# Performance work log

Hardware: AMD Instinct MI355X
Metric: run time of the kernel (lower is better)

Reference implementation:

```python
import jax, jax.numpy as jnp
import numpy as np


def setup_inputs() -> dict:
    key = jax.random.key(0)
    k1, k2, k3 = jax.random.split(key, 3)
    B, n, d = 8, 2048, 128
    x = jax.random.normal(k1, (B, n, d), dtype=jnp.float32)
    adj = jax.random.uniform(k2, (B, n, n), dtype=jnp.float32)
    # nn.Linear(2*d, 1): weight [1, 2d], bias [1]. Store weight flat [2d], bias scalar.
    bound = 1.0 / np.sqrt(2 * d)
    W = jax.random.uniform(k3, (2 * d,), dtype=jnp.float32, minval=-bound, maxval=bound)
    b = jnp.zeros((), dtype=jnp.float32)
    return {"x": x, "adj": adj, "W": W, "b": b}


def reference(x, adj, W, b):
    # linear(cat(x_i, x_j)) == x_i @ W_left + x_j @ W_right + b
    d = x.shape[-1]
    w_left, w_right = W[:d], W[d:]
    s_left = jnp.einsum('bnd,d->bn', x, w_left)   # [B, n]
    s_right = jnp.einsum('bnd,d->bn', x, w_right)  # [B, n]
    att = jax.nn.sigmoid(s_left[:, :, None] + s_right[:, None, :] + b)  # [B, n, n]
    return att * adj
```

## Files before the change

kernel.cpp:

```cpp
#include <hip/hip_runtime.h>
#include <math.h>

#define BATCH 8
#define NN 2048
#define DD 128

__global__ __launch_bounds__(256) void score_kernel(
    const float* __restrict__ x, const float* __restrict__ W,
    const float* __restrict__ bias,
    float* __restrict__ sl, float* __restrict__ sr) {
    int wave = (blockIdx.x * blockDim.x + threadIdx.x) >> 6;
    int lane = threadIdx.x & 63;
    if (wave >= BATCH * NN) return;
    const float* xr = x + (size_t)wave * DD;
    float x0 = xr[lane];
    float x1 = xr[lane + 64];
    float l = x0 * W[lane] + x1 * W[lane + 64];
    float r = x0 * W[DD + lane] + x1 * W[DD + lane + 64];
    #pragma unroll
    for (int off = 32; off; off >>= 1) {
        l += __shfl_xor(l, off, 64);
        r += __shfl_xor(r, off, 64);
    }
    if (lane == 0) {
        sl[wave] = l + bias[0];
        sr[wave] = r;
    }
}

__global__ __launch_bounds__(256) void att_kernel(
    const float* __restrict__ adj, const float* __restrict__ sl,
    const float* __restrict__ sr, float* __restrict__ out) {
    const long total = (long)BATCH * NN * (NN / 4);
    long stride = (long)gridDim.x * blockDim.x;
    for (long e = (long)blockIdx.x * blockDim.x + threadIdx.x; e < total; e += stride) {
        long row = e >> 9;
        int j4 = ((int)e & 511) << 2;
        int b  = (int)(row >> 11);
        float slv = sl[row];
        const float4 s4 = *(const float4*)(sr + (size_t)b * NN + j4);
        const float4 a  = *(const float4*)(adj + ((size_t)row * NN + j4));
        float4 o;
        o.x = a.x / (1.0f + __expf(-(slv + s4.x)));
        o.y = a.y / (1.0f + __expf(-(slv + s4.y)));
        o.z = a.z / (1.0f + __expf(-(slv + s4.z)));
        o.w = a.w / (1.0f + __expf(-(slv + s4.w)));
        *(float4*)(out + ((size_t)row * NN + j4)) = o;
    }
}

extern "C" void kernel_launch(void* const* d_in, const int* in_sizes, int n_in,
                              void* d_out, int out_size, void* d_ws, size_t ws_size,
                              hipStream_t stream) {
    const float* x   = (const float*)d_in[0];
    const float* adj = (const float*)d_in[1];
    const float* W   = (const float*)d_in[2];
    const float* b   = (const float*)d_in[3];
    float* out = (float*)d_out;

    float* sl = (float*)d_ws;
    float* sr = sl + BATCH * NN;

    int rows = BATCH * NN;
    int blocks1 = rows / 4;
    score_kernel<<<blocks1, 256, 0, stream>>>(x, W, b, sl, sr);

    int blocks2 = 2048;
    att_kernel<<<blocks2, 256, 0, stream>>>(adj, sl, sr, out);
}
```

Measured before the change: 58.25 us.

## Restructure attention kernel to fixed 8-row blocks with nontemporal loads/stores and rcp

Replaces the grid-stride loop with one block per 8 rows, each thread handling two float4 per row with unrolled loops, which removes 64-bit index arithmetic and raises memory-level parallelism. Loads of adj and stores of out use nontemporal hints so the streaming data does not pollute the cache. The division is replaced by a hardware reciprocal multiply. The grid grows from 2048 to 2048 blocks of fixed work, and the fast reciprocal gives slightly lower precision.

```diff
diff --git a/kernel.cpp b/kernel.cpp
--- a/kernel.cpp
+++ b/kernel.cpp
@@ -4,6 +4,8 @@
 #define BATCH 8
 #define NN 2048
 #define DD 128
+
+typedef float vf4 __attribute__((ext_vector_type(4)));
 
 __global__ __launch_bounds__(256) void score_kernel(
     const float* __restrict__ x, const float* __restrict__ W,
@@ -31,21 +33,28 @@
 __global__ __launch_bounds__(256) void att_kernel(
     const float* __restrict__ adj, const float* __restrict__ sl,
     const float* __restrict__ sr, float* __restrict__ out) {
-    const long total = (long)BATCH * NN * (NN / 4);
-    long stride = (long)gridDim.x * blockDim.x;
-    for (long e = (long)blockIdx.x * blockDim.x + threadIdx.x; e < total; e += stride) {
-        long row = e >> 9;
-        int j4 = ((int)e & 511) << 2;
-        int b  = (int)(row >> 11);
-        float slv = sl[row];
-        const float4 s4 = *(const float4*)(sr + (size_t)b * NN + j4);
-        const float4 a  = *(const float4*)(adj + ((size_t)row * NN + j4));
-        float4 o;
-        o.x = a.x / (1.0f + __expf(-(slv + s4.x)));
-        o.y = a.y / (1.0f + __expf(-(slv + s4.y)));
-        o.z = a.z / (1.0f + __expf(-(slv + s4.z)));
-        o.w = a.w / (1.0f + __expf(-(slv + s4.w)));
-        *(float4*)(out + ((size_t)row * NN + j4)) = o;
+    const int row0 = blockIdx.x * 8;
+    const int b = row0 >> 11;
+    const vf4* srb = (const vf4*)(sr + (size_t)b * NN);
+    const int tid = threadIdx.x;
+    #pragma unroll
+    for (int r = 0; r < 8; ++r) {
+        const size_t row = row0 + r;
+        const float slv = sl[row];
+        const vf4* arow = (const vf4*)(adj + row * NN);
+        vf4* orow = (vf4*)(out + row * NN);
+        #pragma unroll
+        for (int h = 0; h < 2; ++h) {
+            const int j4 = h * 256 + tid;
+            const vf4 s4 = srb[j4];
+            const vf4 a = __builtin_nontemporal_load(arow + j4);
+            vf4 o;
+            o.x = a.x * __builtin_amdgcn_rcpf(1.0f + __expf(-(slv + s4.x)));
+            o.y = a.y * __builtin_amdgcn_rcpf(1.0f + __expf(-(slv + s4.y)));
+            o.z = a.z * __builtin_amdgcn_rcpf(1.0f + __expf(-(slv + s4.z)));
+            o.w = a.w * __builtin_amdgcn_rcpf(1.0f + __expf(-(slv + s4.w)));
+            __builtin_nontemporal_store(o, orow + j4);
+        }
     }
 }
 
@@ -65,6 +74,5 @@
     int blocks1 = rows / 4;
     score_kernel<<<blocks1, 256, 0, stream>>>(x, W, b, sl, sr);
 
-    int blocks2 = 2048;
-    att_kernel<<<blocks2, 256, 0, stream>>>(adj, sl, sr, out);
+    att_kernel<<<BATCH * NN / 8, 256, 0, stream>>>(adj, sl, sr, out);
 }
```

Result: faster. 55.33 us (-5.0%).
